# Kernel optimization log

Hardware: AMD Instinct MI355X
Metric: run time of the kernel (lower is better)

The kernel has to match this reference:

```python
import jax, jax.numpy as jnp
import numpy as np

D = 128        # node_state_dim
F = 10         # len(CHOSEN_CONNECTION_FEATURES)
N_IP = 20000
N_CONN = 100000
E = 200000
T = 3


def _seg_mean(vals, ids, n):
    s = jax.ops.segment_sum(vals, ids, num_segments=n)
    c = jax.ops.segment_sum(jnp.ones((vals.shape[0], 1), vals.dtype), ids, num_segments=n)
    return s / jnp.maximum(c, 1.0)


def _gru(x, h, kernel, rec_kernel, bias):
    # keras GRUCell, reset_after=True, gate order [z, r, hh]
    xm = x @ kernel + bias[0]
    hm = h @ rec_kernel + bias[1]
    xz, xr, xh = jnp.split(xm, 3, axis=-1)
    hz, hr, hh = jnp.split(hm, 3, axis=-1)
    z = jax.nn.sigmoid(xz + hz)
    r = jax.nn.sigmoid(xr + hr)
    hcand = jnp.tanh(xh + r * hh)
    return z * h + (1.0 - z) * hcand


def setup_inputs() -> dict:
    key = jax.random.key(0)
    ks = jax.random.split(key, 24)
    s = 0.02
    inp = {
        "feature_connection": jax.random.normal(ks[0], (N_CONN, F), jnp.float32),
        "src_ip_to_connection": jax.random.randint(ks[1], (E,), 0, N_IP, jnp.int32),
        "dst_ip_to_connection": jax.random.randint(ks[2], (E,), 0, N_CONN, jnp.int32),
        "src_connection_to_ip": jax.random.randint(ks[3], (E,), 0, N_CONN, jnp.int32),
        "dst_connection_to_ip": jax.random.randint(ks[4], (E,), 0, N_IP, jnp.int32),
        # message MLPs
        "W_m1": jax.random.normal(ks[5], (2 * D, D), jnp.float32) * s,
        "b_m1": jnp.zeros((D,), jnp.float32),
        "W_m2": jax.random.normal(ks[6], (2 * D, D), jnp.float32) * s,
        "b_m2": jnp.zeros((D,), jnp.float32),
        # GRU cells
        "gru_ip_k": jax.random.normal(ks[7], (D, 3 * D), jnp.float32) * s,
        "gru_ip_r": jax.random.normal(ks[8], (D, 3 * D), jnp.float32) * s,
        "gru_ip_b": jnp.zeros((2, 3 * D), jnp.float32),
        "gru_c_k": jax.random.normal(ks[9], (D, 3 * D), jnp.float32) * s,
        "gru_c_r": jax.random.normal(ks[10], (D, 3 * D), jnp.float32) * s,
        "gru_c_b": jnp.zeros((2, 3 * D), jnp.float32),
        # readout MLP
        "W_r1": jax.random.normal(ks[11], (D, 128), jnp.float32) * s,
        "b_r1": jnp.zeros((128,), jnp.float32),
        "W_r2": jax.random.normal(ks[12], (128, 64), jnp.float32) * s,
        "b_r2": jnp.zeros((64,), jnp.float32),
        "W_r3": jax.random.normal(ks[13], (64, 15), jnp.float32) * s,
        "b_r3": jnp.zeros((15,), jnp.float32),
    }
    return inp


def reference(feature_connection, src_ip_to_connection, dst_ip_to_connection,
              src_connection_to_ip, dst_connection_to_ip,
              W_m1, b_m1, W_m2, b_m2,
              gru_ip_k, gru_ip_r, gru_ip_b,
              gru_c_k, gru_c_r, gru_c_b,
              W_r1, b_r1, W_r2, b_r2, W_r3, b_r3):
    ip_state = jnp.ones((N_IP, D), jnp.float32)
    connection_state = jnp.concatenate(
        [feature_connection, jnp.zeros((N_CONN, D - F), jnp.float32)], axis=1)

    for _ in range(T):
        # ip -> connection messages
        nn_in = jnp.concatenate([ip_state[src_ip_to_connection],
                                 connection_state[dst_ip_to_connection]], axis=1)
        ip_message = jax.nn.relu(nn_in @ W_m1 + b_m1)            # [E, D]
        ip_mean = _seg_mean(ip_message, dst_ip_to_connection, N_CONN)
        # connection -> ip messages
        nn_in2 = jnp.concatenate([connection_state[src_connection_to_ip],
                                  ip_state[dst_connection_to_ip]], axis=1)
        conn_message = jax.nn.relu(nn_in2 @ W_m2 + b_m2)         # [E, D]
        conn_mean = _seg_mean(conn_message, dst_connection_to_ip, N_IP)
        # GRU updates
        ip_state = _gru(conn_mean, ip_state, gru_ip_k, gru_ip_r, gru_ip_b)
        connection_state = _gru(ip_mean, connection_state, gru_c_k, gru_c_r, gru_c_b)

    h = jax.nn.relu(connection_state @ W_r1 + b_r1)
    h = jax.nn.relu(h @ W_r2 + b_r2)
    return jax.nn.softmax(h @ W_r3 + b_r3, axis=-1)              # [N_CONN, 15]
```

## Files before the change

kernel.cpp:

```cpp
#include <hip/hip_runtime.h>
#include <math.h>

#define D 128
#define NF 10
#define N_IP 20000
#define N_CONN 100000
#define NE 200000
#define T_ROUNDS 3

typedef unsigned short u16;
using bf16x8 = __attribute__((ext_vector_type(8))) short;
using floatx4 = __attribute__((ext_vector_type(4))) float;

__device__ inline u16 f2bf(float f) {
  union { float f; unsigned u; } v; v.f = f;
  unsigned u = v.u;
  return (u16)((u + 0x7fffu + ((u >> 16) & 1u)) >> 16);
}
__device__ inline float bf2f(u16 h) {
  union { unsigned u; float f; } v; v.u = ((unsigned)h) << 16; return v.f;
}

__device__ inline float fsigmoid(float s) { return 1.f / (1.f + __expf(-s)); }
__device__ inline float ftanh(float a) {
  a = fminf(fmaxf(a, -15.f), 15.f);
  float e = __expf(2.f * a);
  return (e - 1.f) / (e + 1.f);
}

__global__ void k_init_all(u16* __restrict__ ip_state, u16* __restrict__ conn_state,
                           const float* __restrict__ feat, int* __restrict__ cnt) {
  int i = blockIdx.x * blockDim.x + threadIdx.x;
  const int nip = N_IP * D;
  const int nstate = (N_IP + N_CONN) * D;
  if (i < nip) {
    ip_state[i] = 0x3F80;
  } else if (i < nstate) {
    int j = i - nip;
    int r = j >> 7, c = j & 127;
    conn_state[j] = (c < NF) ? f2bf(feat[r * NF + c]) : (u16)0;
  }
  if (i < N_CONN + N_IP) cnt[i] = 0;
}

__global__ void k_prep_all(
    const float* __restrict__ gik, const float* __restrict__ gir,
    const float* __restrict__ gck, const float* __restrict__ gcr,
    const float* __restrict__ Wm1, const float* __restrict__ Wm2,
    const float* __restrict__ Wr1, const float* __restrict__ Wr2,
    u16* __restrict__ gikb, u16* __restrict__ girb,
    u16* __restrict__ gckb, u16* __restrict__ gcrb,
    u16* __restrict__ wm1b, u16* __restrict__ wm2b,
    u16* __restrict__ wm1t, u16* __restrict__ wm2t,
    u16* __restrict__ wr1b, u16* __restrict__ wr2b) {
  int i = blockIdx.x * blockDim.x + threadIdx.x;
  if (i < 196608) {
    int m = i / 49152, r = i % 49152;
    const float* W = (m == 0) ? gik : (m == 1) ? gir : (m == 2) ? gck : gcr;
    u16* Wb = (m == 0) ? gikb : (m == 1) ? girb : (m == 2) ? gckb : gcrb;
    int col = r >> 7, k = r & 127;
    Wb[r] = f2bf(W[k * 384 + col]);
  } else if (i < 278528) {
    int j = i - 196608;
    int m = j / 16384, r = j % 16384;
    const float* W; u16* Wb; int k0;
    if (m == 0) { W = Wm1; Wb = wm1b; k0 = 128; }
    else if (m == 1) { W = Wm2; Wb = wm2b; k0 = 128; }
    else if (m == 2) { W = Wm1; Wb = wm1t; k0 = 0; }
    else if (m == 3) { W = Wm2; Wb = wm2t; k0 = 0; }
    else { W = Wr1; Wb = wr1b; k0 = 0; }
    int col = r >> 7, k = r & 127;
    Wb[r] = f2bf(W[(k0 + k) * 128 + col]);
  } else if (i < 286720) {
    int r = i - 278528;
    int col = r >> 7, k = r & 127;
    wr2b[r] = f2bf(Wr2[k * 64 + col]);
  }
}

__global__ void k_count(const int* __restrict__ d1, const int* __restrict__ d2,
                        int* __restrict__ c1, int* __restrict__ c2) {
  int e = blockIdx.x * blockDim.x + threadIdx.x;
  if (e >= NE) return;
  atomicAdd(&c1[d1[e]], 1);
  atomicAdd(&c2[d2[e]], 1);
}

__global__ void k_scan_part2(const int* __restrict__ cnt1, int* __restrict__ bsum1,
                             int n1, int nb1,
                             const int* __restrict__ cnt2, int* __restrict__ bsum2, int n2) {
  const int* cnt; int* bsum; int n, b;
  if ((int)blockIdx.x < nb1) { cnt = cnt1; bsum = bsum1; n = n1; b = blockIdx.x; }
  else { cnt = cnt2; bsum = bsum2; n = n2; b = blockIdx.x - nb1; }
  int t = threadIdx.x;
  int base = b * 1024 + t * 4;
  int s = 0;
#pragma unroll
  for (int i = 0; i < 4; i++) { int j = base + i; if (j < n) s += cnt[j]; }
  for (int d = 32; d > 0; d >>= 1) s += __shfl_xor(s, d, 64);
  __shared__ int wred[4];
  int lane = t & 63, wv = t >> 6;
  if (lane == 0) wred[wv] = s;
  __syncthreads();
  if (t == 0) bsum[b] = wred[0] + wred[1] + wred[2] + wred[3];
}

__device__ inline void scan_mid_body(int* bsum, int m, int t) {
  int v = (t < m) ? bsum[t] : 0;
  int lane = t & 63, wv = t >> 6;
  int x = v;
  for (int d = 1; d < 64; d <<= 1) { int y = __shfl_up(x, d, 64); if (lane >= d) x += y; }
  __shared__ int wsum[4];
  if (lane == 63) wsum[wv] = x;
  __syncthreads();
  int add = 0;
  for (int i = 0; i < wv; i++) add += wsum[i];
  int ex = add + x - v;
  if (t < m) bsum[t] = ex;
  __syncthreads();
}

__global__ void k_scan_mid2(int* __restrict__ bsum1, int m1, int* __restrict__ bsum2, int m2) {
  int t = threadIdx.x;
  scan_mid_body(bsum1, m1, t);
  scan_mid_body(bsum2, m2, t);
}

__global__ void k_scan_final2(const int* __restrict__ cnt1, const int* __restrict__ bsum1,
                              int* __restrict__ off1, int* __restrict__ cur1, int n1, int nb1,
                              const int* __restrict__ cnt2, const int* __restrict__ bsum2,
                              int* __restrict__ off2, int* __restrict__ cur2, int n2) {
  const int* cnt; const int* bsum; int* off; int* cur; int n, b;
  if ((int)blockIdx.x < nb1) {
    cnt = cnt1; bsum = bsum1; off = off1; cur = cur1; n = n1; b = blockIdx.x;
  } else {
    cnt = cnt2; bsum = bsum2; off = off2; cur = cur2; n = n2; b = blockIdx.x - nb1;
  }
  int t = threadIdx.x;
  int base = b * 1024 + t * 4;
  int vals[4]; int s = 0;
#pragma unroll
  for (int i = 0; i < 4; i++) {
    int j = base + i;
    vals[i] = (j < n) ? cnt[j] : 0;
    s += vals[i];
  }
  int lane = t & 63, wv = t >> 6;
  int x = s;
  for (int d = 1; d < 64; d <<= 1) { int y = __shfl_up(x, d, 64); if (lane >= d) x += y; }
  __shared__ int wsum[4];
  if (lane == 63) wsum[wv] = x;
  __syncthreads();
  int add = 0;
  for (int i = 0; i < wv; i++) add += wsum[i];
  int run = add + x - s + bsum[b];
#pragma unroll
  for (int i = 0; i < 4; i++) {
    int j = base + i;
    if (j < n) { off[j] = run; cur[j] = run; }
    run += vals[i];
  }
}

__global__ void k_scatter(const int* __restrict__ s1, const int* __restrict__ d1,
                          const int* __restrict__ s2, const int* __restrict__ d2,
                          int* __restrict__ cur1, int* __restrict__ cur2,
                          int* __restrict__ o1, int* __restrict__ o2) {
  int e = blockIdx.x * blockDim.x + threadIdx.x;
  if (e >= NE) return;
  int p1 = atomicAdd(&cur1[d1[e]], 1);
  o1[p1] = s1[e];
  int p2 = atomicAdd(&cur2[d2[e]], 1);
  o2[p2] = s2[e];
}

__global__ __launch_bounds__(256) void k_gemmP(
    const u16* __restrict__ S1, const u16* __restrict__ Wt1, u16* __restrict__ P1,
    int M1, int tiles1,
    const u16* __restrict__ S2, const u16* __restrict__ Wt2, u16* __restrict__ P2,
    int M2) {
  __shared__ __align__(16) u16 Wls[128 * 128];
  const u16* S; const u16* Wt; u16* P; int M, bm;
  if ((int)blockIdx.x < tiles1) { S = S1; Wt = Wt1; P = P1; M = M1; bm = blockIdx.x * 128; }
  else { S = S2; Wt = Wt2; P = P2; M = M2; bm = (blockIdx.x - tiles1) * 128; }
  const int tid = threadIdx.x, wv = tid >> 6, lane = tid & 63;
  const int lrow = lane & 15, quad = lane >> 4;
#pragma unroll
  for (int i = 0; i < 8; i++) {
    int task = i * 256 + tid;
    int col = task >> 4, gr = task & 15;
    uint4 v = *(const uint4*)(Wt + (size_t)col * 128 + gr * 8);
    *(uint4*)(Wls + (size_t)col * 128 + ((gr ^ (col & 15)) * 8)) = v;
  }
  const bf16x8 zv = {0, 0, 0, 0, 0, 0, 0, 0};
  bf16x8 a[2][4];
#pragma unroll
  for (int tile = 0; tile < 2; tile++) {
    int arow = bm + tile * 64 + wv * 16 + lrow;
    bool arv = arow < M;
#pragma unroll
    for (int ks = 0; ks < 4; ks++)
      a[tile][ks] = arv ? *(const bf16x8*)(S + (size_t)arow * 128 + quad * 8 + ks * 32) : zv;
  }
  __syncthreads();
  floatx4 acc[2][8];
#pragma unroll
  for (int tile = 0; tile < 2; tile++)
#pragma unroll
    for (int ct = 0; ct < 8; ct++) acc[tile][ct] = {0.f, 0.f, 0.f, 0.f};
#pragma unroll
  for (int ks = 0; ks < 4; ks++) {
#pragma unroll
    for (int ct = 0; ct < 8; ct++) {
      int col = ct * 16 + lrow;
      bf16x8 b = *(const bf16x8*)(Wls + (size_t)col * 128 + (((4 * ks + quad) ^ lrow) * 8));
      acc[0][ct] = __builtin_amdgcn_mfma_f32_16x16x32_bf16(a[0][ks], b, acc[0][ct], 0, 0, 0);
      acc[1][ct] = __builtin_amdgcn_mfma_f32_16x16x32_bf16(a[1][ks], b, acc[1][ct], 0, 0, 0);
    }
  }
  u16* Cls = Wls;
#pragma unroll
  for (int tile = 0; tile < 2; tile++) {
    __syncthreads();
#pragma unroll
    for (int ct = 0; ct < 8; ct++) {
      int col = ct * 16 + lrow;
#pragma unroll
      for (int reg = 0; reg < 4; reg++) {
        int lr = wv * 16 + quad * 4 + reg;
        Cls[(size_t)lr * 136 + col] = f2bf(acc[tile][ct][reg]);
      }
    }
    __syncthreads();
#pragma unroll
    for (int i = 0; i < 4; i++) {
      int task = i * 256 + tid;
      int row = task >> 4, c8 = task & 15;
      int gr2 = bm + tile * 64 + row;
      if (gr2 < M)
        *(uint4*)(P + (size_t)gr2 * 128 + c8 * 8) =
            *(const uint4*)(Cls + (size_t)row * 136 + c8 * 8);
    }
  }
}

__global__ __launch_bounds__(256, 3) void k_msggru(
    u16* __restrict__ st1, const u16* __restrict__ wq1, const float* __restrict__ qb1,
    const u16* __restrict__ P1g, const int* __restrict__ srcs1g,
    const int* __restrict__ off1g, const int* __restrict__ cnt1g,
    const u16* __restrict__ wx1, const u16* __restrict__ wh1, const float* __restrict__ gb1,
    int r1, int tiles1,
    u16* __restrict__ st2, const u16* __restrict__ wq2, const float* __restrict__ qb2,
    const u16* __restrict__ P2g, const int* __restrict__ srcs2g,
    const int* __restrict__ off2g, const int* __restrict__ cnt2g,
    const u16* __restrict__ wx2, const u16* __restrict__ wh2, const float* __restrict__ gb2,
    int r2) {
  __shared__ __align__(16) char smem[49152];
  __shared__ int offLs[64];
  __shared__ int cntLs[64];
  u16* Wq = (u16*)smem;
  u16* Qb = (u16*)smem;
  u16* Xb = (u16*)(smem + 16384);
  u16* Wg = (u16*)smem;
  u16* Hls = (u16*)(smem + 32768);
  u16* H; const u16* Wqb; const float* qbias; const u16* P;
  const int* srcs; const int* off; const int* cnt;
  const u16* Wxb; const u16* Whb; const float* gbias; int rows, bm;
  if ((int)blockIdx.x < tiles1) {
    H = st1; Wqb = wq1; qbias = qb1; P = P1g; srcs = srcs1g; off = off1g; cnt = cnt1g;
    Wxb = wx1; Whb = wh1; gbias = gb1; rows = r1; bm = blockIdx.x * 64;
  } else {
    H = st2; Wqb = wq2; qbias = qb2; P = P2g; srcs = srcs2g; off = off2g; cnt = cnt2g;
    Wxb = wx2; Whb = wh2; gbias = gb2; rows = r2; bm = (blockIdx.x - tiles1) * 64;
  }
  const int tid = threadIdx.x, wv = tid >> 6, lane = tid & 63;
  const int lrow = lane & 15, quad = lane >> 4;
  const uint4 z4 = {0, 0, 0, 0};
#pragma unroll
  for (int i = 0; i < 8; i++) {
    int task = i * 256 + tid;
    int col = task >> 4, gr = task & 15;
    uint4 v = *(const uint4*)(Wqb + (size_t)col * 128 + gr * 8);
    *(uint4*)(Wq + (size_t)col * 128 + ((gr ^ (col & 15)) * 8)) = v;
  }
#pragma unroll
  for (int i = 0; i < 4; i++) {
    int task = i * 256 + tid;
    int row = task >> 4, g = task & 15;
    int grow = bm + row;
    uint4 v = (grow < rows) ? *(const uint4*)(H + (size_t)grow * 128 + g * 8) : z4;
    *(uint4*)(Hls + (size_t)row * 128 + ((g ^ (row & 15)) * 8)) = v;
  }
  if (tid < 64) {
    int node = bm + tid;
    offLs[tid] = (node < rows) ? off[node] : 0;
    cntLs[tid] = (node < rows) ? cnt[node] : 0;
  }
  __syncthreads();
  bf16x8 ah[4];
#pragma unroll
  for (int ks = 0; ks < 4; ks++)
    ah[ks] = *(const bf16x8*)(Hls + (size_t)(wv * 16 + lrow) * 128 + (((ks * 4 + quad) ^ lrow) * 8));
  floatx4 acc[8];
#pragma unroll
  for (int ct = 0; ct < 8; ct++) acc[ct] = {0.f, 0.f, 0.f, 0.f};
#pragma unroll
  for (int ks = 0; ks < 4; ks++) {
#pragma unroll
    for (int ct = 0; ct < 8; ct++) {
      int col = ct * 16 + lrow;
      bf16x8 b = *(const bf16x8*)(Wq + (size_t)col * 128 + (((4 * ks + quad) ^ lrow) * 8));
      acc[ct] = __builtin_amdgcn_mfma_f32_16x16x32_bf16(ah[ks], b, acc[ct], 0, 0, 0);
    }
  }
  __syncthreads();
#pragma unroll
  for (int ct = 0; ct < 8; ct++) {
    int col = ct * 16 + lrow;
    float bv = qbias[col];
#pragma unroll
    for (int reg = 0; reg < 4; reg++) {
      int lr = wv * 16 + quad * 4 + reg;
      Qb[(size_t)lr * 128 + col] = f2bf(acc[ct][reg] + bv);
    }
  }
  __syncthreads();
#pragma unroll
  for (int it = 0; it < 4; it++) {
    int task = it * 256 + tid;
    int nl = task >> 4, g = task & 15;
    int node = bm + nl;
    if (node >= rows) continue;
    int c8 = g << 3;
    float q[8];
    {
      uint4 qv = *(const uint4*)(Qb + (size_t)nl * 128 + c8);
      unsigned qq[4] = {qv.x, qv.y, qv.z, qv.w};
#pragma unroll
      for (int k = 0; k < 4; k++) {
        q[2 * k] = __uint_as_float(qq[k] << 16);
        q[2 * k + 1] = __uint_as_float(qq[k] & 0xffff0000u);
      }
    }
    float acg[8] = {0.f, 0.f, 0.f, 0.f, 0.f, 0.f, 0.f, 0.f};
    int o = offLs[nl], n = cntLs[nl];
    int i = 0;
    for (; i + 4 <= n; i += 4) {
      int s0 = srcs[o + i], s1 = srcs[o + i + 1], s2 = srcs[o + i + 2], s3 = srcs[o + i + 3];
      uint4 v0 = *(const uint4*)(P + (size_t)s0 * 128 + c8);
      uint4 v1 = *(const uint4*)(P + (size_t)s1 * 128 + c8);
      uint4 v2 = *(const uint4*)(P + (size_t)s2 * 128 + c8);
      uint4 v3 = *(const uint4*)(P + (size_t)s3 * 128 + c8);
      unsigned w[16] = {v0.x, v0.y, v0.z, v0.w, v1.x, v1.y, v1.z, v1.w,
                        v2.x, v2.y, v2.z, v2.w, v3.x, v3.y, v3.z, v3.w};
#pragma unroll
      for (int e = 0; e < 4; e++)
#pragma unroll
        for (int k = 0; k < 4; k++) {
          unsigned ww = w[e * 4 + k];
          float lo = __uint_as_float(ww << 16);
          float hi = __uint_as_float(ww & 0xffff0000u);
          acg[2 * k] += fmaxf(lo + q[2 * k], 0.f);
          acg[2 * k + 1] += fmaxf(hi + q[2 * k + 1], 0.f);
        }
    }
    for (; i < n; i++) {
      int s0 = srcs[o + i];
      uint4 v0 = *(const uint4*)(P + (size_t)s0 * 128 + c8);
      unsigned w[4] = {v0.x, v0.y, v0.z, v0.w};
#pragma unroll
      for (int k = 0; k < 4; k++) {
        unsigned ww = w[k];
        float lo = __uint_as_float(ww << 16);
        float hi = __uint_as_float(ww & 0xffff0000u);
        acg[2 * k] += fmaxf(lo + q[2 * k], 0.f);
        acg[2 * k + 1] += fmaxf(hi + q[2 * k + 1], 0.f);
      }
    }
    float inv = 1.f / fmaxf((float)n, 1.f);
    bf16x8 ov;
#pragma unroll
    for (int k = 0; k < 8; k++) ov[k] = (short)f2bf(acg[k] * inv);
    *(bf16x8*)(Xb + (size_t)nl * 128 + ((g ^ (nl & 15)) * 8)) = ov;
  }
  __syncthreads();
  bf16x8 ax[4];
#pragma unroll
  for (int ks = 0; ks < 4; ks++)
    ax[ks] = *(const bf16x8*)(Xb + (size_t)(wv * 16 + lrow) * 128 + (((ks * 4 + quad) ^ lrow) * 8));
  const int lr0 = wv * 16 + quad * 4;
  const u16* gp0; const u16* gp1; const u16* gp2;
  const u16* gp3; const u16* gp4; const u16* gp5;
  u16* lp0; u16* lp1; u16* lp2; u16* lp3; u16* lp4; u16* lp5;
  {
#define MK_PTRS(J, GP, LP)                                                      \
    {                                                                           \
      int task = (J) * 256 + tid;                                               \
      int seg = task >> 8, rem = task & 255;                                    \
      int col = rem >> 4, gr = rem & 15;                                        \
      GP = (seg < 3 ? Wxb : Whb) +                                              \
           (size_t)((seg < 3 ? seg : seg - 3) * 128 + col) * 128 + gr * 8;      \
      LP = Wg + (size_t)(seg * 16 + col) * 128 + ((gr ^ col) * 8);              \
    }
    MK_PTRS(0, gp0, lp0) MK_PTRS(1, gp1, lp1) MK_PTRS(2, gp2, lp2)
    MK_PTRS(3, gp3, lp3) MK_PTRS(4, gp4, lp4) MK_PTRS(5, gp5, lp5)
#undef MK_PTRS
  }
  uint4 v0 = *(const uint4*)(gp0);
  uint4 v1 = *(const uint4*)(gp1);
  uint4 v2 = *(const uint4*)(gp2);
  uint4 v3 = *(const uint4*)(gp3);
  uint4 v4 = *(const uint4*)(gp4);
  uint4 v5 = *(const uint4*)(gp5);
  for (int ch = 0; ch < 8; ch++) {
    __syncthreads();
    *(uint4*)lp0 = v0; *(uint4*)lp1 = v1; *(uint4*)lp2 = v2;
    *(uint4*)lp3 = v3; *(uint4*)lp4 = v4; *(uint4*)lp5 = v5;
    __syncthreads();
    if (ch < 7) {
      size_t d = (size_t)(ch + 1) * 2048;
      v0 = *(const uint4*)(gp0 + d);
      v1 = *(const uint4*)(gp1 + d);
      v2 = *(const uint4*)(gp2 + d);
      v3 = *(const uint4*)(gp3 + d);
      v4 = *(const uint4*)(gp4 + d);
      v5 = *(const uint4*)(gp5 + d);
    }
    floatx4 gacc[3][2];
#pragma unroll
    for (int g = 0; g < 3; g++) {
      gacc[g][0] = {0.f, 0.f, 0.f, 0.f};
      gacc[g][1] = {0.f, 0.f, 0.f, 0.f};
    }
#pragma unroll
    for (int ks = 0; ks < 4; ks++) {
      int posu = ((4 * ks + quad) ^ lrow) * 8;
#pragma unroll
      for (int g = 0; g < 3; g++) {
        bf16x8 bx = *(const bf16x8*)(Wg + (size_t)(g * 16 + lrow) * 128 + posu);
        bf16x8 bh = *(const bf16x8*)(Wg + (size_t)((3 + g) * 16 + lrow) * 128 + posu);
        gacc[g][0] = __builtin_amdgcn_mfma_f32_16x16x32_bf16(ax[ks], bx, gacc[g][0], 0, 0, 0);
        gacc[g][1] = __builtin_amdgcn_mfma_f32_16x16x32_bf16(ah[ks], bh, gacc[g][1], 0, 0, 0);
      }
    }
    int hcol = ch * 16 + lrow;
    float bxz = gbias[hcol];
    float bxr = gbias[128 + hcol];
    float bxh = gbias[256 + hcol];
    float bhz = gbias[384 + hcol];
    float bhr = gbias[384 + 128 + hcol];
    float bhh = gbias[384 + 256 + hcol];
    int ggr = 2 * ch + (lrow >> 3);
    int gel = lrow & 7;
#pragma unroll
    for (int reg = 0; reg < 4; reg++) {
      int lr = lr0 + reg;
      float xz = gacc[0][0][reg] + bxz;
      float xr = gacc[1][0][reg] + bxr;
      float xh = gacc[2][0][reg] + bxh;
      float hz = gacc[0][1][reg] + bhz;
      float hr = gacc[1][1][reg] + bhr;
      float hh = gacc[2][1][reg] + bhh;
      float z = fsigmoid(xz + hz);
      float rr = fsigmoid(xr + hr);
      float hc = ftanh(xh + rr * hh);
      u16* hp = Hls + (size_t)lr * 128 + ((ggr ^ (lr & 15)) * 8) + gel;
      float hold = bf2f(*hp);
      *hp = f2bf(z * hold + (1.f - z) * hc);
    }
  }
  __syncthreads();
#pragma unroll
  for (int i = 0; i < 4; i++) {
    int task = i * 256 + tid;
    int row = task >> 4, g = task & 15;
    int grow = bm + row;
    if (grow < rows)
      *(uint4*)(H + (size_t)grow * 128 + g * 8) =
          *(const uint4*)(Hls + (size_t)row * 128 + ((g ^ (row & 15)) * 8));
  }
}

__global__ __launch_bounds__(256) void k_readout2(
    const u16* __restrict__ S, const u16* __restrict__ W1b, const float* __restrict__ b1,
    const u16* __restrict__ W2b, const float* __restrict__ b2,
    const float* __restrict__ W3, const float* __restrict__ b3,
    float* __restrict__ out, int M) {
  __shared__ __align__(16) char smem[64 * 132 * 4];
  u16* Wls = (u16*)smem;
  u16* H1ls = (u16*)smem;
  u16* W2ls = (u16*)(smem + 17408);
  u16* H2ls = (u16*)smem;
  float* W3ls = (float*)(smem + 9216);
  float* b3ls = (float*)(smem + 9216 + 3840);
  const int tid = threadIdx.x, wv = tid >> 6, lane = tid & 63;
  const int lrow = lane & 15, quad = lane >> 4;
  const int bm = blockIdx.x * 64;
#pragma unroll
  for (int i = 0; i < 8; i++) {
    int task = i * 256 + tid;
    int col = task >> 4, gr = task & 15;
    uint4 v = *(const uint4*)(W1b + (size_t)col * 128 + gr * 8);
    *(uint4*)(Wls + (size_t)col * 128 + ((gr ^ (col & 15)) * 8)) = v;
  }
  const int arow = bm + wv * 16 + lrow;
  const bool arv = arow < M;
  const bf16x8 zv = {0, 0, 0, 0, 0, 0, 0, 0};
  bf16x8 a[4];
#pragma unroll
  for (int ks = 0; ks < 4; ks++)
    a[ks] = arv ? *(const bf16x8*)(S + (size_t)arow * 128 + quad * 8 + ks * 32) : zv;
  __syncthreads();
  floatx4 acc1[8];
#pragma unroll
  for (int ct = 0; ct < 8; ct++) acc1[ct] = {0.f, 0.f, 0.f, 0.f};
#pragma unroll
  for (int ks = 0; ks < 4; ks++) {
#pragma unroll
    for (int ct = 0; ct < 8; ct++) {
      int col = ct * 16 + lrow;
      bf16x8 b = *(const bf16x8*)(Wls + (size_t)col * 128 + (((4 * ks + quad) ^ lrow) * 8));
      acc1[ct] = __builtin_amdgcn_mfma_f32_16x16x32_bf16(a[ks], b, acc1[ct], 0, 0, 0);
    }
  }
  __syncthreads();
#pragma unroll
  for (int ct = 0; ct < 8; ct++) {
    int col = ct * 16 + lrow;
    float bv = b1[col];
#pragma unroll
    for (int reg = 0; reg < 4; reg++) {
      int lr = wv * 16 + quad * 4 + reg;
      H1ls[(size_t)lr * 136 + col] = f2bf(fmaxf(acc1[ct][reg] + bv, 0.f));
    }
  }
#pragma unroll
  for (int i = 0; i < 4; i++) {
    int task = i * 256 + tid;
    int col = task >> 4, gr = task & 15;
    uint4 v = *(const uint4*)(W2b + (size_t)col * 128 + gr * 8);
    *(uint4*)(W2ls + (size_t)col * 128 + ((gr ^ (col & 15)) * 8)) = v;
  }
  __syncthreads();
  bf16x8 a2[4];
#pragma unroll
  for (int ks = 0; ks < 4; ks++)
    a2[ks] = *(const bf16x8*)(H1ls + (size_t)(wv * 16 + lrow) * 136 + quad * 8 + ks * 32);
  floatx4 acc2[4];
#pragma unroll
  for (int ct = 0; ct < 4; ct++) acc2[ct] = {0.f, 0.f, 0.f, 0.f};
#pragma unroll
  for (int ks = 0; ks < 4; ks++) {
#pragma unroll
    for (int ct = 0; ct < 4; ct++) {
      int col = ct * 16 + lrow;
      bf16x8 b = *(const bf16x8*)(W2ls + (size_t)col * 128 + (((4 * ks + quad) ^ lrow) * 8));
      acc2[ct] = __builtin_amdgcn_mfma_f32_16x16x32_bf16(a2[ks], b, acc2[ct], 0, 0, 0);
    }
  }
  __syncthreads();
#pragma unroll
  for (int ct = 0; ct < 4; ct++) {
    int col = ct * 16 + lrow;
    float bv = b2[col];
#pragma unroll
    for (int reg = 0; reg < 4; reg++) {
      int lr = wv * 16 + quad * 4 + reg;
      H2ls[(size_t)lr * 72 + col] = f2bf(fmaxf(acc2[ct][reg] + bv, 0.f));
    }
  }
  for (int l = tid; l < 960; l += 256) W3ls[l] = W3[l];
  if (tid < 15) b3ls[tid] = b3[tid];
  __syncthreads();
  if (tid < 64) {
    int row = tid, gr2 = bm + row;
    if (gr2 < M) {
      float lg[15];
#pragma unroll
      for (int c = 0; c < 15; c++) lg[c] = b3ls[c];
      for (int k = 0; k < 64; k++) {
        float hk = bf2f(H2ls[(size_t)row * 72 + k]);
#pragma unroll
        for (int c = 0; c < 15; c++) lg[c] += hk * W3ls[k * 15 + c];
      }
      float m = lg[0];
#pragma unroll
      for (int c = 1; c < 15; c++) m = fmaxf(m, lg[c]);
      float ssum = 0.f;
#pragma unroll
      for (int c = 0; c < 15; c++) { lg[c] = __expf(lg[c] - m); ssum += lg[c]; }
      float inv = 1.f / ssum;
#pragma unroll
      for (int c = 0; c < 15; c++) out[(size_t)gr2 * 15 + c] = lg[c] * inv;
    }
  }
}

extern "C" void kernel_launch(void* const* d_in, const int* in_sizes, int n_in,
                              void* d_out, int out_size, void* d_ws, size_t ws_size,
                              hipStream_t stream) {
  const float* feat = (const float*)d_in[0];
  const int* src1 = (const int*)d_in[1];
  const int* dst1 = (const int*)d_in[2];
  const int* src2 = (const int*)d_in[3];
  const int* dst2 = (const int*)d_in[4];
  const float* Wm1 = (const float*)d_in[5];
  const float* bm1 = (const float*)d_in[6];
  const float* Wm2 = (const float*)d_in[7];
  const float* bm2 = (const float*)d_in[8];
  const float* gik = (const float*)d_in[9];
  const float* gir = (const float*)d_in[10];
  const float* gib = (const float*)d_in[11];
  const float* gck = (const float*)d_in[12];
  const float* gcr = (const float*)d_in[13];
  const float* gcb = (const float*)d_in[14];
  const float* Wr1 = (const float*)d_in[15];
  const float* br1 = (const float*)d_in[16];
  const float* Wr2 = (const float*)d_in[17];
  const float* br2 = (const float*)d_in[18];
  const float* Wr3 = (const float*)d_in[19];
  const float* br3 = (const float*)d_in[20];
  float* out = (float*)d_out;

  u16* w16 = (u16*)d_ws;
  size_t o = 0;
  u16* ip_state = w16 + o;   o += (size_t)N_IP * D;
  u16* conn_state = w16 + o; o += (size_t)N_CONN * D;
  u16* P1 = w16 + o;         o += (size_t)N_IP * D;
  u16* P2 = w16 + o;         o += (size_t)N_CONN * D;
  u16* gikb = w16 + o;       o += 49152;
  u16* girb = w16 + o;       o += 49152;
  u16* gckb = w16 + o;       o += 49152;
  u16* gcrb = w16 + o;       o += 49152;
  u16* wm1b = w16 + o;       o += 16384;
  u16* wm2b = w16 + o;       o += 16384;
  u16* wm1t = w16 + o;       o += 16384;
  u16* wm2t = w16 + o;       o += 16384;
  u16* wr1b = w16 + o;       o += 16384;
  u16* wr2b = w16 + o;       o += 8192;
  int* ip = (int*)(w16 + o);
  int* cnt1 = ip;  ip += N_CONN;
  int* cnt2 = ip;  ip += N_IP;
  int* off1 = ip;  ip += N_CONN;
  int* off2 = ip;  ip += N_IP;
  int* cur1 = ip;  ip += N_CONN;
  int* cur2 = ip;  ip += N_IP;
  int* srcs1 = ip; ip += NE;
  int* srcs2 = ip; ip += NE;
  int* bsum1 = ip; ip += 256;
  int* bsum2 = ip; ip += 256;

  const int BT = 256;

  const int nstate = (N_IP + N_CONN) * D;
  k_init_all<<<(nstate + BT - 1) / BT, BT, 0, stream>>>(ip_state, conn_state, feat, cnt1);
  k_prep_all<<<(286720 + BT - 1) / BT, BT, 0, stream>>>(
      gik, gir, gck, gcr, Wm1, Wm2, Wr1, Wr2,
      gikb, girb, gckb, gcrb, wm1b, wm2b, wm1t, wm2t, wr1b, wr2b);

  k_count<<<(NE + BT - 1) / BT, BT, 0, stream>>>(dst1, dst2, cnt1, cnt2);
  const int nb1 = (N_CONN + 1023) / 1024, nb2 = (N_IP + 1023) / 1024;
  k_scan_part2<<<nb1 + nb2, 256, 0, stream>>>(cnt1, bsum1, N_CONN, nb1, cnt2, bsum2, N_IP);
  k_scan_mid2<<<1, 256, 0, stream>>>(bsum1, nb1, bsum2, nb2);
  k_scan_final2<<<nb1 + nb2, 256, 0, stream>>>(cnt1, bsum1, off1, cur1, N_CONN, nb1,
                                               cnt2, bsum2, off2, cur2, N_IP);
  k_scatter<<<(NE + BT - 1) / BT, BT, 0, stream>>>(src1, dst1, src2, dst2,
                                                   cur1, cur2, srcs1, srcs2);

  const int t64ip = (N_IP + 63) / 64;
  const int t64cn = (N_CONN + 63) / 64;
  const int t128ip = (N_IP + 127) / 128;
  const int t128cn = (N_CONN + 127) / 128;

  for (int t = 0; t < T_ROUNDS; t++) {
    k_gemmP<<<t128ip + t128cn, 256, 0, stream>>>(ip_state, wm1t, P1, N_IP, t128ip,
                                                 conn_state, wm2t, P2, N_CONN);
    k_msggru<<<t64cn + t64ip, 256, 0, stream>>>(
        conn_state, wm1b, bm1, P1, srcs1, off1, cnt1, gckb, gcrb, gcb, N_CONN, t64cn,
        ip_state, wm2b, bm2, P2, srcs2, off2, cnt2, gikb, girb, gib, N_IP);
  }

  k_readout2<<<t64cn, 256, 0, stream>>>(conn_state, wr1b, br1, wr2b, br2,
                                        Wr3, br3, out, N_CONN);
}
```

Baseline: 511.6 us.

## Fuse projection GEMM into GRU kernel epilogue and compute initial projections analytically

Removes the separate k_gemmP launch per round. Each k_msggru block now multiplies its freshly updated state tile by the message weight and writes the next round's projection P into a double buffer, reusing the state already in shared memory. The first round's projections come from closed forms: a column sum of Wm1 for the all-ones ip state, and the 10 features times Wm2 for connections. The cost is more shared-memory work and register pressure in the GRU kernel, plus a second pair of P buffers.

```diff
diff --git a/kernel.cpp b/kernel.cpp
--- a/kernel.cpp
+++ b/kernel.cpp
@@ -78,6 +78,43 @@
   }
 }
 
+__global__ void k_colsum(const float* __restrict__ Wm1, float* __restrict__ csum) {
+  int c = threadIdx.x;
+  float s = 0.f;
+  for (int k = 0; k < 128; k++) s += Wm1[k * 128 + c];
+  csum[c] = s;
+}
+
+__global__ void k_initP(const float* __restrict__ csum, const float* __restrict__ feat,
+                        const float* __restrict__ Wm2,
+                        u16* __restrict__ P1, u16* __restrict__ P2) {
+  int i = blockIdx.x * blockDim.x + threadIdx.x;
+  const int n1 = N_IP * 16;
+  const int n2 = N_CONN * 16;
+  if (i < n1) {
+    int r = i >> 4, g = i & 15;
+    u16 v[8];
+#pragma unroll
+    for (int k = 0; k < 8; k++) v[k] = f2bf(csum[g * 8 + k]);
+    *(uint4*)(P1 + (size_t)r * 128 + g * 8) = *(const uint4*)v;
+  } else if (i < n1 + n2) {
+    int j = i - n1;
+    int r = j >> 4, g = j & 15;
+    float acc[8] = {0.f, 0.f, 0.f, 0.f, 0.f, 0.f, 0.f, 0.f};
+#pragma unroll
+    for (int k = 0; k < NF; k++) {
+      float f = feat[(size_t)r * NF + k];
+      const float* wrow = Wm2 + (size_t)k * 128 + g * 8;
+#pragma unroll
+      for (int c = 0; c < 8; c++) acc[c] += f * wrow[c];
+    }
+    u16 v[8];
+#pragma unroll
+    for (int c = 0; c < 8; c++) v[c] = f2bf(acc[c]);
+    *(uint4*)(P2 + (size_t)r * 128 + g * 8) = *(const uint4*)v;
+  }
+}
+
 __global__ void k_count(const int* __restrict__ d1, const int* __restrict__ d2,
                         int* __restrict__ c1, int* __restrict__ c2) {
   int e = blockIdx.x * blockDim.x + threadIdx.x;
@@ -174,87 +211,17 @@
   o2[p2] = s2[e];
 }
 
-__global__ __launch_bounds__(256) void k_gemmP(
-    const u16* __restrict__ S1, const u16* __restrict__ Wt1, u16* __restrict__ P1,
-    int M1, int tiles1,
-    const u16* __restrict__ S2, const u16* __restrict__ Wt2, u16* __restrict__ P2,
-    int M2) {
-  __shared__ __align__(16) u16 Wls[128 * 128];
-  const u16* S; const u16* Wt; u16* P; int M, bm;
-  if ((int)blockIdx.x < tiles1) { S = S1; Wt = Wt1; P = P1; M = M1; bm = blockIdx.x * 128; }
-  else { S = S2; Wt = Wt2; P = P2; M = M2; bm = (blockIdx.x - tiles1) * 128; }
-  const int tid = threadIdx.x, wv = tid >> 6, lane = tid & 63;
-  const int lrow = lane & 15, quad = lane >> 4;
-#pragma unroll
-  for (int i = 0; i < 8; i++) {
-    int task = i * 256 + tid;
-    int col = task >> 4, gr = task & 15;
-    uint4 v = *(const uint4*)(Wt + (size_t)col * 128 + gr * 8);
-    *(uint4*)(Wls + (size_t)col * 128 + ((gr ^ (col & 15)) * 8)) = v;
-  }
-  const bf16x8 zv = {0, 0, 0, 0, 0, 0, 0, 0};
-  bf16x8 a[2][4];
-#pragma unroll
-  for (int tile = 0; tile < 2; tile++) {
-    int arow = bm + tile * 64 + wv * 16 + lrow;
-    bool arv = arow < M;
-#pragma unroll
-    for (int ks = 0; ks < 4; ks++)
-      a[tile][ks] = arv ? *(const bf16x8*)(S + (size_t)arow * 128 + quad * 8 + ks * 32) : zv;
-  }
-  __syncthreads();
-  floatx4 acc[2][8];
-#pragma unroll
-  for (int tile = 0; tile < 2; tile++)
-#pragma unroll
-    for (int ct = 0; ct < 8; ct++) acc[tile][ct] = {0.f, 0.f, 0.f, 0.f};
-#pragma unroll
-  for (int ks = 0; ks < 4; ks++) {
-#pragma unroll
-    for (int ct = 0; ct < 8; ct++) {
-      int col = ct * 16 + lrow;
-      bf16x8 b = *(const bf16x8*)(Wls + (size_t)col * 128 + (((4 * ks + quad) ^ lrow) * 8));
-      acc[0][ct] = __builtin_amdgcn_mfma_f32_16x16x32_bf16(a[0][ks], b, acc[0][ct], 0, 0, 0);
-      acc[1][ct] = __builtin_amdgcn_mfma_f32_16x16x32_bf16(a[1][ks], b, acc[1][ct], 0, 0, 0);
-    }
-  }
-  u16* Cls = Wls;
-#pragma unroll
-  for (int tile = 0; tile < 2; tile++) {
-    __syncthreads();
-#pragma unroll
-    for (int ct = 0; ct < 8; ct++) {
-      int col = ct * 16 + lrow;
-#pragma unroll
-      for (int reg = 0; reg < 4; reg++) {
-        int lr = wv * 16 + quad * 4 + reg;
-        Cls[(size_t)lr * 136 + col] = f2bf(acc[tile][ct][reg]);
-      }
-    }
-    __syncthreads();
-#pragma unroll
-    for (int i = 0; i < 4; i++) {
-      int task = i * 256 + tid;
-      int row = task >> 4, c8 = task & 15;
-      int gr2 = bm + tile * 64 + row;
-      if (gr2 < M)
-        *(uint4*)(P + (size_t)gr2 * 128 + c8 * 8) =
-            *(const uint4*)(Cls + (size_t)row * 136 + c8 * 8);
-    }
-  }
-}
-
 __global__ __launch_bounds__(256, 3) void k_msggru(
     u16* __restrict__ st1, const u16* __restrict__ wq1, const float* __restrict__ qb1,
     const u16* __restrict__ P1g, const int* __restrict__ srcs1g,
     const int* __restrict__ off1g, const int* __restrict__ cnt1g,
     const u16* __restrict__ wx1, const u16* __restrict__ wh1, const float* __restrict__ gb1,
-    int r1, int tiles1,
+    const u16* __restrict__ wp1, u16* __restrict__ Pn1, int r1, int tiles1,
     u16* __restrict__ st2, const u16* __restrict__ wq2, const float* __restrict__ qb2,
     const u16* __restrict__ P2g, const int* __restrict__ srcs2g,
     const int* __restrict__ off2g, const int* __restrict__ cnt2g,
     const u16* __restrict__ wx2, const u16* __restrict__ wh2, const float* __restrict__ gb2,
-    int r2) {
+    const u16* __restrict__ wp2, u16* __restrict__ Pn2, int r2, int doP) {
   __shared__ __align__(16) char smem[49152];
   __shared__ int offLs[64];
   __shared__ int cntLs[64];
@@ -265,13 +232,15 @@
   u16* Hls = (u16*)(smem + 32768);
   u16* H; const u16* Wqb; const float* qbias; const u16* P;
   const int* srcs; const int* off; const int* cnt;
-  const u16* Wxb; const u16* Whb; const float* gbias; int rows, bm;
+  const u16* Wxb; const u16* Whb; const float* gbias;
+  const u16* Wpt; u16* Pn; int rows, bm;
   if ((int)blockIdx.x < tiles1) {
     H = st1; Wqb = wq1; qbias = qb1; P = P1g; srcs = srcs1g; off = off1g; cnt = cnt1g;
-    Wxb = wx1; Whb = wh1; gbias = gb1; rows = r1; bm = blockIdx.x * 64;
+    Wxb = wx1; Whb = wh1; gbias = gb1; Wpt = wp1; Pn = Pn1; rows = r1; bm = blockIdx.x * 64;
   } else {
     H = st2; Wqb = wq2; qbias = qb2; P = P2g; srcs = srcs2g; off = off2g; cnt = cnt2g;
-    Wxb = wx2; Whb = wh2; gbias = gb2; rows = r2; bm = (blockIdx.x - tiles1) * 64;
+    Wxb = wx2; Whb = wh2; gbias = gb2; Wpt = wp2; Pn = Pn2; rows = r2;
+    bm = (blockIdx.x - tiles1) * 64;
   }
   const int tid = threadIdx.x, wv = tid >> 6, lane = tid & 63;
   const int lrow = lane & 15, quad = lane >> 4;
@@ -478,6 +447,51 @@
     if (grow < rows)
       *(uint4*)(H + (size_t)grow * 128 + g * 8) =
           *(const uint4*)(Hls + (size_t)row * 128 + ((g ^ (row & 15)) * 8));
+  }
+  if (!doP) return;
+  bf16x8 ah2[4];
+#pragma unroll
+  for (int ks = 0; ks < 4; ks++)
+    ah2[ks] = *(const bf16x8*)(Hls + (size_t)(wv * 16 + lrow) * 128 + (((ks * 4 + quad) ^ lrow) * 8));
+  u16* Wp = (u16*)smem;
+#pragma unroll
+  for (int i = 0; i < 8; i++) {
+    int task = i * 256 + tid;
+    int col = task >> 4, gr = task & 15;
+    uint4 v = *(const uint4*)(Wpt + (size_t)col * 128 + gr * 8);
+    *(uint4*)(Wp + (size_t)col * 128 + ((gr ^ (col & 15)) * 8)) = v;
+  }
+  __syncthreads();
+#pragma unroll
+  for (int ct = 0; ct < 8; ct++) acc[ct] = {0.f, 0.f, 0.f, 0.f};
+#pragma unroll
+  for (int ks = 0; ks < 4; ks++) {
+#pragma unroll
+    for (int ct = 0; ct < 8; ct++) {
+      int col = ct * 16 + lrow;
+      bf16x8 b = *(const bf16x8*)(Wp + (size_t)col * 128 + (((4 * ks + quad) ^ lrow) * 8));
+      acc[ct] = __builtin_amdgcn_mfma_f32_16x16x32_bf16(ah2[ks], b, acc[ct], 0, 0, 0);
+    }
+  }
+  u16* Cls = Hls;
+#pragma unroll
+  for (int ct = 0; ct < 8; ct++) {
+    int col = ct * 16 + lrow;
+#pragma unroll
+    for (int reg = 0; reg < 4; reg++) {
+      int lr = wv * 16 + quad * 4 + reg;
+      Cls[(size_t)lr * 128 + col] = f2bf(acc[ct][reg]);
+    }
+  }
+  __syncthreads();
+#pragma unroll
+  for (int i = 0; i < 4; i++) {
+    int task = i * 256 + tid;
+    int row = task >> 4, g = task & 15;
+    int grow = bm + row;
+    if (grow < rows)
+      *(uint4*)(Pn + (size_t)grow * 128 + g * 8) =
+          *(const uint4*)(Cls + (size_t)row * 128 + g * 8);
   }
 }
 
@@ -626,8 +640,10 @@
   size_t o = 0;
   u16* ip_state = w16 + o;   o += (size_t)N_IP * D;
   u16* conn_state = w16 + o; o += (size_t)N_CONN * D;
-  u16* P1 = w16 + o;         o += (size_t)N_IP * D;
-  u16* P2 = w16 + o;         o += (size_t)N_CONN * D;
+  u16* P1a = w16 + o;        o += (size_t)N_IP * D;
+  u16* P2a = w16 + o;        o += (size_t)N_CONN * D;
+  u16* P1b = w16 + o;        o += (size_t)N_IP * D;
+  u16* P2b = w16 + o;        o += (size_t)N_CONN * D;
   u16* gikb = w16 + o;       o += 49152;
   u16* girb = w16 + o;       o += 49152;
   u16* gckb = w16 + o;       o += 49152;
@@ -638,6 +654,7 @@
   u16* wm2t = w16 + o;       o += 16384;
   u16* wr1b = w16 + o;       o += 16384;
   u16* wr2b = w16 + o;       o += 8192;
+  float* csum = (float*)(w16 + o); o += 256;
   int* ip = (int*)(w16 + o);
   int* cnt1 = ip;  ip += N_CONN;
   int* cnt2 = ip;  ip += N_IP;
@@ -657,6 +674,9 @@
   k_prep_all<<<(286720 + BT - 1) / BT, BT, 0, stream>>>(
       gik, gir, gck, gcr, Wm1, Wm2, Wr1, Wr2,
       gikb, girb, gckb, gcrb, wm1b, wm2b, wm1t, wm2t, wr1b, wr2b);
+  k_colsum<<<1, 128, 0, stream>>>(Wm1, csum);
+  const int nPinit = (N_IP + N_CONN) * 16;
+  k_initP<<<(nPinit + BT - 1) / BT, BT, 0, stream>>>(csum, feat, Wm2, P1a, P2a);
 
   k_count<<<(NE + BT - 1) / BT, BT, 0, stream>>>(dst1, dst2, cnt1, cnt2);
   const int nb1 = (N_CONN + 1023) / 1024, nb2 = (N_IP + 1023) / 1024;
@@ -669,15 +689,16 @@
 
   const int t64ip = (N_IP + 63) / 64;
   const int t64cn = (N_CONN + 63) / 64;
-  const int t128ip = (N_IP + 127) / 128;
-  const int t128cn = (N_CONN + 127) / 128;
-
+
+  u16* P1buf[2] = {P1a, P1b};
+  u16* P2buf[2] = {P2a, P2b};
   for (int t = 0; t < T_ROUNDS; t++) {
-    k_gemmP<<<t128ip + t128cn, 256, 0, stream>>>(ip_state, wm1t, P1, N_IP, t128ip,
-                                                 conn_state, wm2t, P2, N_CONN);
-    k_msggru<<<t64cn + t64ip, 256, 0, stream>>>(
-        conn_state, wm1b, bm1, P1, srcs1, off1, cnt1, gckb, gcrb, gcb, N_CONN, t64cn,
-        ip_state, wm2b, bm2, P2, srcs2, off2, cnt2, gikb, girb, gib, N_IP);
+    int cu = t & 1, nx = cu ^ 1;
+    k_msggru<<<t64ip + t64cn, 256, 0, stream>>>(
+        ip_state, wm2b, bm2, P2buf[cu], srcs2, off2, cnt2, gikb, girb, gib,
+        wm1t, P1buf[nx], N_IP, t64ip,
+        conn_state, wm1b, bm1, P1buf[cu], srcs1, off1, cnt1, gckb, gcrb, gcb,
+        wm2t, P2buf[nx], N_CONN, (t < T_ROUNDS - 1) ? 1 : 0);
   }
 
   k_readout2<<<t64cn, 256, 0, stream>>>(conn_state, wr1b, br1, wr2b, br2,
```

New measurement: 493.3 us. 3.6% less time.
